# Performance work log

Measured on AMD Instinct MI355X. Metric: run time of the kernel, lower is better.

## Reference

```python
import jax, jax.numpy as jnp
import numpy as np


def setup_inputs() -> dict:
    key = jax.random.key(0)
    k1, k2 = jax.random.split(key)
    b, f, H, W = 16, 16, 304, 608
    stimuli = jax.random.normal(k1, (b, f, H, W), dtype=jnp.float32)
    eye = jax.random.normal(k2, (b, f, 6), dtype=jnp.float32)
    return {"stimuli": stimuli, "eye": eye}


def _make_grid(H, W):
    # Normalized sampling grid with homogeneous coordinate: (3, H*W)
    x_t = jnp.linspace(-1.0, 1.0, W, dtype=jnp.float32)
    y_t = jnp.linspace(-1.0, 1.0, H, dtype=jnp.float32)
    xg, yg = jnp.meshgrid(x_t, y_t)  # each (H, W)
    ones = jnp.ones((H * W,), dtype=jnp.float32)
    return jnp.stack([xg.reshape(-1), yg.reshape(-1), ones], axis=0)


def reference(stimuli, eye):
    b, f, H, W = stimuli.shape
    HW = H * W
    grid = _make_grid(H, W)  # (3, HW)

    affines = eye.reshape(b, f, 2, 3).astype(jnp.float32)
    # T_g: transformed sampling coords, (b, f, 2, HW)
    T_g = jnp.einsum('bfij,jp->bfip', affines, grid)
    x = T_g[:, :, 0, :]  # (b, f, HW)
    y = T_g[:, :, 1, :]

    Wf = jnp.float32(W)
    Hf = jnp.float32(H)
    x = (x + 1.0) * Wf / 2.0
    y = (y + 1.0) * Hf / 2.0

    x0 = jnp.floor(x).astype(jnp.int32)
    x1 = x0 + 1
    y0 = jnp.floor(y).astype(jnp.int32)
    y1 = y0 + 1
    x0 = jnp.clip(x0, 0, W - 1)
    x1 = jnp.clip(x1, 0, W - 1)
    y0 = jnp.clip(y0, 0, H - 1)
    y1 = jnp.clip(y1, 0, H - 1)

    imf = stimuli.reshape(b, f, HW).astype(jnp.float32)
    # Four corner gathers (channel dim is 1 -> elided)
    Ia = jnp.take_along_axis(imf, y0 * W + x0, axis=-1)
    Ib = jnp.take_along_axis(imf, y1 * W + x0, axis=-1)
    Ic = jnp.take_along_axis(imf, y0 * W + x1, axis=-1)
    Id = jnp.take_along_axis(imf, y1 * W + x1, axis=-1)

    x0f = x0.astype(jnp.float32)
    x1f = x1.astype(jnp.float32)
    y0f = y0.astype(jnp.float32)
    y1f = y1.astype(jnp.float32)
    wa = (x1f - x) * (y1f - y)
    wb = (x1f - x) * (y - y0f)
    wc = (x - x0f) * (y1f - y)
    wd = (x - x0f) * (y - y0f)

    out = wa * Ia + wb * Ib + wc * Ic + wd * Id  # (b, f, HW)
    return out.reshape(b, f, H, W)
```

## Files before the change

### kernel.cpp

```cpp
#include <hip/hip_runtime.h>
#include <math.h>

#define IMG_H 304
#define IMG_W 608
#define IMG_HW (IMG_H * IMG_W)
#define TPB 128

#define TILE 16
#define TILES_X (IMG_W / TILE)
#define TILES_Y (IMG_H / TILE)
#define NTILES (TILES_X * TILES_Y)
#define TILES_PER_BLOCK 2

typedef float f2u __attribute__((ext_vector_type(2), aligned(4)));
typedef float f4v __attribute__((ext_vector_type(4)));

__global__ __launch_bounds__(TPB) void grid_sample_kernel(
    const float* __restrict__ stimuli,
    const float* __restrict__ eye,
    float* __restrict__ out)
{
    #pragma clang fp contract(off)

    const int bf = blockIdx.y;
    const float* __restrict__ img = stimuli + (size_t)bf * IMG_HW;
    float* __restrict__ o = out + (size_t)bf * IMG_HW;

    const float a0 = eye[bf * 6 + 0];
    const float a1 = eye[bf * 6 + 1];
    const float a2 = eye[bf * 6 + 2];
    const float a3 = eye[bf * 6 + 3];
    const float a4 = eye[bf * 6 + 4];
    const float a5 = eye[bf * 6 + 5];

    const int wave = threadIdx.x >> 6;
    const int lane = threadIdx.x & 63;
    const int t = blockIdx.x * TILES_PER_BLOCK + wave;
    const int tile_r = t / TILES_X;
    const int tile_c = t - tile_r * TILES_X;
    const int row = tile_r * TILE + (lane >> 2);
    const int col = tile_c * TILE + ((lane & 3) << 2);

    float yg;
    if (row == IMG_H - 1) {
        yg = 1.0f;
    } else {
        const float ty = (float)row / 303.0f;
        yg = ty - (1.0f - ty);
    }

    float res[4];
#pragma unroll
    for (int i = 0; i < 4; ++i) {
        const int j = col + i;
        float xg;
        if (j == IMG_W - 1) {
            xg = 1.0f;
        } else {
            const float tx = (float)j / 607.0f;
            xg = tx - (1.0f - tx);
        }

        const float xs = fmaf(a1, yg, a0 * xg) + a2;
        const float ys = fmaf(a4, yg, a3 * xg) + a5;

        const float x = ((xs + 1.0f) * (float)IMG_W) / 2.0f;
        const float y = ((ys + 1.0f) * (float)IMG_H) / 2.0f;

        const float fx0 = floorf(x);
        const float fy0 = floorf(y);
        const int x0 = (int)fx0;
        const int y0 = (int)fy0;

        const int x0c = min(max(x0, 0), IMG_W - 1);
        const int x1c = min(max(x0 + 1, 0), IMG_W - 1);
        const int y0c = min(max(y0, 0), IMG_H - 1);
        const int y1c = min(max(y0 + 1, 0), IMG_H - 1);

        const int xp = min(x0c, IMG_W - 2);
        const f2u ra = *reinterpret_cast<const f2u*>(img + y0c * IMG_W + xp);
        const f2u rb = *reinterpret_cast<const f2u*>(img + y1c * IMG_W + xp);

        const bool hi = (x0 >= IMG_W - 1);
        const bool lo = (x0 < 0);
        const float Ia = hi ? ra.y : ra.x;
        const float Ic = lo ? ra.x : ra.y;
        const float Ib = hi ? rb.y : rb.x;
        const float Id = lo ? rb.x : rb.y;

        const float x0f = (float)x0c, x1f = (float)x1c;
        const float y0f = (float)y0c, y1f = (float)y1c;

        const float wxa = x1f - x;
        const float wxb = x - x0f;
        const float wya = y1f - y;
        const float wyb = y - y0f;

        const float wa = wxa * wya;
        const float wb = wxa * wyb;
        const float wc = wxb * wya;
        const float wd = wxb * wyb;

        const float s0 = (wa * Ia) + (wb * Ib);
        const float s1 = s0 + (wc * Ic);
        res[i] = s1 + (wd * Id);
    }

    f4v v = { res[0], res[1], res[2], res[3] };
    __builtin_nontemporal_store(
        v, reinterpret_cast<f4v*>(o + (size_t)row * IMG_W + col));
}

extern "C" void kernel_launch(void* const* d_in, const int* in_sizes, int n_in,
                              void* d_out, int out_size, void* d_ws, size_t ws_size,
                              hipStream_t stream) {
    const float* stimuli = (const float*)d_in[0];
    const float* eye     = (const float*)d_in[1];
    float* out           = (float*)d_out;

    const int n_imgs = in_sizes[1] / 6;
    const int blocks_x = NTILES / TILES_PER_BLOCK;
    dim3 grid(blocks_x, n_imgs);
    grid_sample_kernel<<<grid, TPB, 0, stream>>>(stimuli, eye, out);
}
```

Before: 357.5 us.

## Precompute grid coords in shared memory and remap tile to 8x8 subtile lanes

Per-column x-grid products and per-row y-grid values are computed once per tile by a subset of lanes and staged in shared memory behind a barrier. The per-lane mapping also changes from 4 adjacent columns per lane to an 8x8 square per wave iteration. The square layout is meant to give better gather locality under a spatial transform. In exchange, the float4 nontemporal store becomes four scalar stores of 32 bytes per row, and a block-wide sync is added.

```diff
diff --git a/kernel.cpp b/kernel.cpp
--- a/kernel.cpp
+++ b/kernel.cpp
@@ -13,7 +13,6 @@
 #define TILES_PER_BLOCK 2
 
 typedef float f2u __attribute__((ext_vector_type(2), aligned(4)));
-typedef float f4v __attribute__((ext_vector_type(4)));
 
 __global__ __launch_bounds__(TPB) void grid_sample_kernel(
     const float* __restrict__ stimuli,
@@ -21,6 +20,9 @@
     float* __restrict__ out)
 {
     #pragma clang fp contract(off)
+
+    __shared__ float2 s_cx[TILES_PER_BLOCK][TILE];
+    __shared__ float  s_yg[TILES_PER_BLOCK][TILE];
 
     const int bf = blockIdx.y;
     const float* __restrict__ img = stimuli + (size_t)bf * IMG_HW;
@@ -38,21 +40,9 @@
     const int t = blockIdx.x * TILES_PER_BLOCK + wave;
     const int tile_r = t / TILES_X;
     const int tile_c = t - tile_r * TILES_X;
-    const int row = tile_r * TILE + (lane >> 2);
-    const int col = tile_c * TILE + ((lane & 3) << 2);
 
-    float yg;
-    if (row == IMG_H - 1) {
-        yg = 1.0f;
-    } else {
-        const float ty = (float)row / 303.0f;
-        yg = ty - (1.0f - ty);
-    }
-
-    float res[4];
-#pragma unroll
-    for (int i = 0; i < 4; ++i) {
-        const int j = col + i;
+    if (lane < TILE) {
+        const int j = tile_c * TILE + lane;
         float xg;
         if (j == IMG_W - 1) {
             xg = 1.0f;
@@ -60,55 +50,81 @@
             const float tx = (float)j / 607.0f;
             xg = tx - (1.0f - tx);
         }
+        s_cx[wave][lane] = make_float2(a0 * xg, a3 * xg);
+    } else if (lane < 2 * TILE) {
+        const int r = lane - TILE;
+        const int rr = tile_r * TILE + r;
+        float yg;
+        if (rr == IMG_H - 1) {
+            yg = 1.0f;
+        } else {
+            const float ty = (float)rr / 303.0f;
+            yg = ty - (1.0f - ty);
+        }
+        s_yg[wave][r] = yg;
+    }
+    __syncthreads();
 
-        const float xs = fmaf(a1, yg, a0 * xg) + a2;
-        const float ys = fmaf(a4, yg, a3 * xg) + a5;
+    const int ry = lane >> 3;
+    const int cx = lane & 7;
 
-        const float x = ((xs + 1.0f) * (float)IMG_W) / 2.0f;
-        const float y = ((ys + 1.0f) * (float)IMG_H) / 2.0f;
+#pragma unroll
+    for (int si = 0; si < 2; ++si) {
+#pragma unroll
+        for (int sj = 0; sj < 2; ++sj) {
+            const int row = tile_r * TILE + si * 8 + ry;
+            const int col = tile_c * TILE + sj * 8 + cx;
 
-        const float fx0 = floorf(x);
-        const float fy0 = floorf(y);
-        const int x0 = (int)fx0;
-        const int y0 = (int)fy0;
+            const float2 c0  = s_cx[wave][sj * 8 + cx];
+            const float  ygv = s_yg[wave][si * 8 + ry];
 
-        const int x0c = min(max(x0, 0), IMG_W - 1);
-        const int x1c = min(max(x0 + 1, 0), IMG_W - 1);
-        const int y0c = min(max(y0, 0), IMG_H - 1);
-        const int y1c = min(max(y0 + 1, 0), IMG_H - 1);
+            const float xs = fmaf(a1, ygv, c0.x) + a2;
+            const float ys = fmaf(a4, ygv, c0.y) + a5;
 
-        const int xp = min(x0c, IMG_W - 2);
-        const f2u ra = *reinterpret_cast<const f2u*>(img + y0c * IMG_W + xp);
-        const f2u rb = *reinterpret_cast<const f2u*>(img + y1c * IMG_W + xp);
+            const float x = ((xs + 1.0f) * (float)IMG_W) / 2.0f;
+            const float y = ((ys + 1.0f) * (float)IMG_H) / 2.0f;
 
-        const bool hi = (x0 >= IMG_W - 1);
-        const bool lo = (x0 < 0);
-        const float Ia = hi ? ra.y : ra.x;
-        const float Ic = lo ? ra.x : ra.y;
-        const float Ib = hi ? rb.y : rb.x;
-        const float Id = lo ? rb.x : rb.y;
+            const float fx0 = floorf(x);
+            const float fy0 = floorf(y);
+            const int x0 = (int)fx0;
+            const int y0 = (int)fy0;
 
-        const float x0f = (float)x0c, x1f = (float)x1c;
-        const float y0f = (float)y0c, y1f = (float)y1c;
+            const int x0c = min(max(x0, 0), IMG_W - 1);
+            const int x1c = min(max(x0 + 1, 0), IMG_W - 1);
+            const int y0c = min(max(y0, 0), IMG_H - 1);
+            const int y1c = min(max(y0 + 1, 0), IMG_H - 1);
 
-        const float wxa = x1f - x;
-        const float wxb = x - x0f;
-        const float wya = y1f - y;
-        const float wyb = y - y0f;
+            const int xp = min(x0c, IMG_W - 2);
+            const f2u ra = *reinterpret_cast<const f2u*>(img + y0c * IMG_W + xp);
+            const f2u rb = *reinterpret_cast<const f2u*>(img + y1c * IMG_W + xp);
 
-        const float wa = wxa * wya;
-        const float wb = wxa * wyb;
-        const float wc = wxb * wya;
-        const float wd = wxb * wyb;
+            const bool hi = (x0 >= IMG_W - 1);
+            const bool lo = (x0 < 0);
+            const float Ia = hi ? ra.y : ra.x;
+            const float Ic = lo ? ra.x : ra.y;
+            const float Ib = hi ? rb.y : rb.x;
+            const float Id = lo ? rb.x : rb.y;
 
-        const float s0 = (wa * Ia) + (wb * Ib);
-        const float s1 = s0 + (wc * Ic);
-        res[i] = s1 + (wd * Id);
+            const float x0f = (float)x0c, x1f = (float)x1c;
+            const float y0f = (float)y0c, y1f = (float)y1c;
+
+            const float wxa = x1f - x;
+            const float wxb = x - x0f;
+            const float wya = y1f - y;
+            const float wyb = y - y0f;
+
+            const float wa = wxa * wya;
+            const float wb = wxa * wyb;
+            const float wc = wxb * wya;
+            const float wd = wxb * wyb;
+
+            const float s0 = (wa * Ia) + (wb * Ib);
+            const float s1 = s0 + (wc * Ic);
+            const float rv = s1 + (wd * Id);
+
+            o[(size_t)row * IMG_W + col] = rv;
+        }
     }
-
-    f4v v = { res[0], res[1], res[2], res[3] };
-    __builtin_nontemporal_store(
-        v, reinterpret_cast<f4v*>(o + (size_t)row * IMG_W + col));
 }
 
 extern "C" void kernel_launch(void* const* d_in, const int* in_sizes, int n_in,
```

After: 358.0 us. No clear change (+0.1%).
